# Performance work log

Measured on AMD Instinct MI355X. Metric: run time of the kernel, lower is better.

Reference implementation:

```python
import jax, jax.numpy as jnp
import numpy as np

RESOLUTION = 128


def _bin_mask():
    # [4, 2] bool: corner i, dim d -> True if corner uses floor coord in dim d
    neigs = jnp.arange(4, dtype=jnp.int32)[:, None]
    dims = jnp.arange(2, dtype=jnp.int32)[None, :]
    return (neigs & (1 << dims)) == 0


def setup_inputs() -> dict:
    key = jax.random.key(0)
    k1, k2 = jax.random.split(key)
    batch = 65536
    res, map_num, feat_dim = RESOLUTION, 128, 8
    inputs = jax.random.uniform(k1, (batch, 2), dtype=jnp.float32)
    # xavier_uniform over [res^2, map_num*feat_dim]
    fan_in, fan_out = res * res, map_num * feat_dim
    bound = float(np.sqrt(6.0 / (fan_in + fan_out)))
    embeddings = jax.random.uniform(k2, (res * res, map_num * feat_dim),
                                    dtype=jnp.float32, minval=-bound, maxval=bound)
    return {"inputs": inputs, "embeddings": embeddings}


def reference(inputs, embeddings):
    res = RESOLUTION
    bin_mask = _bin_mask()                      # [4, 2]
    x = inputs * (res - 1)                      # [B, 2]
    xi = jnp.floor(x).astype(jnp.int32)         # [B, 2]
    xf = x - jax.lax.stop_gradient(jnp.floor(x))  # fractional part, grads flow via x
    xi = xi[:, None, :]                         # [B, 1, 2]
    xf = xf[:, None, :]                         # [B, 1, 2]
    neigs = jnp.where(bin_mask, xi, xi + 1)     # [B, 4, 2]
    ids = neigs[..., 0] * res + neigs[..., 1]   # [B, 4]
    neigs_features = embeddings[ids]            # [B, 4, D] irregular gather
    weights = jnp.where(bin_mask, 1.0 - xf, xf) # [B, 4, 2]
    w = jnp.prod(weights, axis=-1, keepdims=True)  # [B, 4, 1]
    return jnp.sum(neigs_features * w, axis=-2)    # [B, D]
```

## Files before the change

kernel.cpp:

```cpp
#include <hip/hip_runtime.h>

#define RES   128
#define FEAT  1024
#define NBINS (RES * RES)

__global__ __launch_bounds__(256)
void hist_kernel(const float* __restrict__ inputs, unsigned* __restrict__ hist, int N)
{
    int p = blockIdx.x * 256 + threadIdx.x;
    if (p >= N) return;
    int i0 = (int)floorf(inputs[2 * p + 0] * (float)(RES - 1));
    int i1 = (int)floorf(inputs[2 * p + 1] * (float)(RES - 1));
    atomicAdd(&hist[i0 * RES + i1], 1u);
}

__global__ __launch_bounds__(256)
void scan_kernel(unsigned* __restrict__ hist)
{
    __shared__ unsigned part[256];
    int t = threadIdx.x;
    int base = t * 64;
    unsigned s = 0;
    for (int k = 0; k < 64; ++k) s += hist[base + k];
    part[t] = s;
    __syncthreads();
    if (t == 0) {
        unsigned run = 0;
        for (int i = 0; i < 256; ++i) { unsigned v = part[i]; part[i] = run; run += v; }
    }
    __syncthreads();
    unsigned run = part[t];
    for (int k = 0; k < 64; ++k) { unsigned v = hist[base + k]; hist[base + k] = run; run += v; }
}

__global__ __launch_bounds__(256)
void scatter_kernel(const float* __restrict__ inputs, unsigned* __restrict__ hist,
                    unsigned* __restrict__ order, int N)
{
    int p = blockIdx.x * 256 + threadIdx.x;
    if (p >= N) return;
    int i0 = (int)floorf(inputs[2 * p + 0] * (float)(RES - 1));
    int i1 = (int)floorf(inputs[2 * p + 1] * (float)(RES - 1));
    unsigned pos = atomicAdd(&hist[i0 * RES + i1], 1u);
    order[pos] = (unsigned)p;
}

__global__ __launch_bounds__(256)
void DenseMap_sorted_kernel(const float* __restrict__ inputs,
                            const float* __restrict__ emb,
                            const unsigned* __restrict__ order,
                            float* __restrict__ out,
                            int N, int chunk)
{
    const int b = blockIdx.x;
    const int c = threadIdx.x;
    const int g = (chunk > 0) ? ((b & 7) * chunk + (b >> 3)) : b;

#pragma unroll
    for (int j = 0; j < 4; ++j) {
        const int s = g * 4 + j;
        if (s >= N) break;
        const int p = (int)order[s];

        const float x0 = inputs[2 * p + 0] * (float)(RES - 1);
        const float x1 = inputs[2 * p + 1] * (float)(RES - 1);
        const float f0 = floorf(x0);
        const float f1 = floorf(x1);
        const int   i0 = (int)f0;
        const int   i1 = (int)f1;
        const float xf0 = x0 - f0;
        const float xf1 = x1 - f1;

        const float w00 = (1.0f - xf0) * (1.0f - xf1);
        const float w01 = (1.0f - xf0) * xf1;
        const float w10 = xf0 * (1.0f - xf1);
        const float w11 = xf0 * xf1;

        const long base = (long)(i0 * RES + i1) * FEAT;
        const float4 a = ((const float4*)(emb + base))[c];
        const float4 bb = ((const float4*)(emb + base + FEAT))[c];
        const float4 gg = ((const float4*)(emb + base + (long)RES * FEAT))[c];
        const float4 h = ((const float4*)(emb + base + (long)RES * FEAT + FEAT))[c];

        float4 r;
        r.x = a.x * w00 + bb.x * w01 + gg.x * w10 + h.x * w11;
        r.y = a.y * w00 + bb.y * w01 + gg.y * w10 + h.y * w11;
        r.z = a.z * w00 + bb.z * w01 + gg.z * w10 + h.z * w11;
        r.w = a.w * w00 + bb.w * w01 + gg.w * w10 + h.w * w11;

        ((float4*)(out + (long)p * FEAT))[c] = r;
    }
}

__global__ __launch_bounds__(256)
void DenseMap_fallback_kernel(const float* __restrict__ inputs,
                              const float* __restrict__ emb,
                              float* __restrict__ out)
{
    const int p = blockIdx.x;
    const int c = threadIdx.x;

    const float x0 = inputs[2 * p + 0] * (float)(RES - 1);
    const float x1 = inputs[2 * p + 1] * (float)(RES - 1);
    const float f0 = floorf(x0);
    const float f1 = floorf(x1);
    const int   i0 = (int)f0;
    const int   i1 = (int)f1;
    const float xf0 = x0 - f0;
    const float xf1 = x1 - f1;

    const float w00 = (1.0f - xf0) * (1.0f - xf1);
    const float w01 = (1.0f - xf0) * xf1;
    const float w10 = xf0 * (1.0f - xf1);
    const float w11 = xf0 * xf1;

    const long base = (long)(i0 * RES + i1) * FEAT;
    const float4 a = ((const float4*)(emb + base))[c];
    const float4 b = ((const float4*)(emb + base + FEAT))[c];
    const float4 g = ((const float4*)(emb + base + (long)RES * FEAT))[c];
    const float4 h = ((const float4*)(emb + base + (long)RES * FEAT + FEAT))[c];

    float4 r;
    r.x = a.x * w00 + b.x * w01 + g.x * w10 + h.x * w11;
    r.y = a.y * w00 + b.y * w01 + g.y * w10 + h.y * w11;
    r.z = a.z * w00 + b.z * w01 + g.z * w10 + h.z * w11;
    r.w = a.w * w00 + b.w * w01 + g.w * w10 + h.w * w11;

    ((float4*)(out + (long)p * FEAT))[c] = r;
}

extern "C" void kernel_launch(void* const* d_in, const int* in_sizes, int n_in,
                              void* d_out, int out_size, void* d_ws, size_t ws_size,
                              hipStream_t stream)
{
    const float* inputs = (const float*)d_in[0];
    const float* emb    = (const float*)d_in[1];
    float*       out    = (float*)d_out;

    const int N = in_sizes[0] / 2;
    const size_t need = (size_t)(NBINS + N) * sizeof(unsigned);

    if (ws_size >= need) {
        unsigned* hist  = (unsigned*)d_ws;
        unsigned* order = hist + NBINS;

        hipMemsetAsync(hist, 0, NBINS * sizeof(unsigned), stream);
        hist_kernel<<<(N + 255) / 256, 256, 0, stream>>>(inputs, hist, N);
        scan_kernel<<<1, 256, 0, stream>>>(hist);
        scatter_kernel<<<(N + 255) / 256, 256, 0, stream>>>(inputs, hist, order, N);

        const int G = (N + 3) / 4;
        const int chunk = (G % 8 == 0) ? (G / 8) : 0;
        DenseMap_sorted_kernel<<<G, 256, 0, stream>>>(inputs, emb, order, out, N, chunk);
    } else {
        DenseMap_fallback_kernel<<<N, 256, 0, stream>>>(inputs, emb, out);
    }
}
```

Baseline: 388.6 us.

## Sort points in Morton order, batch eight points per block, use nontemporal stores

Sort keys change from row-major cell index to a Z-order (Morton) code, so consecutive sorted points are spatially local in both dimensions and reuse more embedding rows in cache. Each block now processes eight points instead of four and computes all indices and weights up front, so several gathers can be in flight at once. Output is written with nontemporal stores so it does not evict embedding lines from cache. The cost is more registers per thread and fewer blocks.

```diff
diff --git a/kernel.cpp b/kernel.cpp
--- a/kernel.cpp
+++ b/kernel.cpp
@@ -3,15 +3,32 @@
 #define RES   128
 #define FEAT  1024
 #define NBINS (RES * RES)
+#define PPB   8
+
+typedef float float4n __attribute__((ext_vector_type(4)));
+
+__device__ __forceinline__ unsigned part1by1(unsigned x)
+{
+    x &= 0x7F;
+    x = (x | (x << 4)) & 0x0F0F;
+    x = (x | (x << 2)) & 0x3333;
+    x = (x | (x << 1)) & 0x5555;
+    return x;
+}
+
+__device__ __forceinline__ unsigned cell_code(const float* __restrict__ inputs, int p)
+{
+    int i0 = (int)floorf(inputs[2 * p + 0] * (float)(RES - 1));
+    int i1 = (int)floorf(inputs[2 * p + 1] * (float)(RES - 1));
+    return (part1by1((unsigned)i0) << 1) | part1by1((unsigned)i1);
+}
 
 __global__ __launch_bounds__(256)
 void hist_kernel(const float* __restrict__ inputs, unsigned* __restrict__ hist, int N)
 {
     int p = blockIdx.x * 256 + threadIdx.x;
     if (p >= N) return;
-    int i0 = (int)floorf(inputs[2 * p + 0] * (float)(RES - 1));
-    int i1 = (int)floorf(inputs[2 * p + 1] * (float)(RES - 1));
-    atomicAdd(&hist[i0 * RES + i1], 1u);
+    atomicAdd(&hist[cell_code(inputs, p)], 1u);
 }
 
 __global__ __launch_bounds__(256)
@@ -39,9 +56,7 @@
 {
     int p = blockIdx.x * 256 + threadIdx.x;
     if (p >= N) return;
-    int i0 = (int)floorf(inputs[2 * p + 0] * (float)(RES - 1));
-    int i1 = (int)floorf(inputs[2 * p + 1] * (float)(RES - 1));
-    unsigned pos = atomicAdd(&hist[i0 * RES + i1], 1u);
+    unsigned pos = atomicAdd(&hist[cell_code(inputs, p)], 1u);
     order[pos] = (unsigned)p;
 }
 
@@ -55,40 +70,45 @@
     const int b = blockIdx.x;
     const int c = threadIdx.x;
     const int g = (chunk > 0) ? ((b & 7) * chunk + (b >> 3)) : b;
+    const int s0 = g * PPB;
+
+    long  base[PPB];
+    float W00[PPB], W01[PPB], W10[PPB], W11[PPB];
+    int   pp[PPB];
 
 #pragma unroll
-    for (int j = 0; j < 4; ++j) {
-        const int s = g * 4 + j;
-        if (s >= N) break;
-        const int p = (int)order[s];
+    for (int j = 0; j < PPB; ++j) {
+        const int s = s0 + j;
+        const int p = (s < N) ? (int)order[s] : -1;
+        pp[j] = p;
+        if (p >= 0) {
+            const float x0 = inputs[2 * p + 0] * (float)(RES - 1);
+            const float x1 = inputs[2 * p + 1] * (float)(RES - 1);
+            const float f0 = floorf(x0);
+            const float f1 = floorf(x1);
+            const float xf0 = x0 - f0;
+            const float xf1 = x1 - f1;
+            base[j] = (long)((int)f0 * RES + (int)f1) * FEAT;
+            W00[j] = (1.0f - xf0) * (1.0f - xf1);
+            W01[j] = (1.0f - xf0) * xf1;
+            W10[j] = xf0 * (1.0f - xf1);
+            W11[j] = xf0 * xf1;
+        }
+    }
 
-        const float x0 = inputs[2 * p + 0] * (float)(RES - 1);
-        const float x1 = inputs[2 * p + 1] * (float)(RES - 1);
-        const float f0 = floorf(x0);
-        const float f1 = floorf(x1);
-        const int   i0 = (int)f0;
-        const int   i1 = (int)f1;
-        const float xf0 = x0 - f0;
-        const float xf1 = x1 - f1;
+#pragma unroll
+    for (int j = 0; j < PPB; ++j) {
+        const int p = pp[j];
+        if (p < 0) continue;
+        const long bs = base[j];
+        const float4n a  = ((const float4n*)(emb + bs))[c];
+        const float4n bb = ((const float4n*)(emb + bs + FEAT))[c];
+        const float4n gg = ((const float4n*)(emb + bs + (long)RES * FEAT))[c];
+        const float4n hh = ((const float4n*)(emb + bs + (long)RES * FEAT + FEAT))[c];
 
-        const float w00 = (1.0f - xf0) * (1.0f - xf1);
-        const float w01 = (1.0f - xf0) * xf1;
-        const float w10 = xf0 * (1.0f - xf1);
-        const float w11 = xf0 * xf1;
+        float4n r = a * W00[j] + bb * W01[j] + gg * W10[j] + hh * W11[j];
 
-        const long base = (long)(i0 * RES + i1) * FEAT;
-        const float4 a = ((const float4*)(emb + base))[c];
-        const float4 bb = ((const float4*)(emb + base + FEAT))[c];
-        const float4 gg = ((const float4*)(emb + base + (long)RES * FEAT))[c];
-        const float4 h = ((const float4*)(emb + base + (long)RES * FEAT + FEAT))[c];
-
-        float4 r;
-        r.x = a.x * w00 + bb.x * w01 + gg.x * w10 + h.x * w11;
-        r.y = a.y * w00 + bb.y * w01 + gg.y * w10 + h.y * w11;
-        r.z = a.z * w00 + bb.z * w01 + gg.z * w10 + h.z * w11;
-        r.w = a.w * w00 + bb.w * w01 + gg.w * w10 + h.w * w11;
-
-        ((float4*)(out + (long)p * FEAT))[c] = r;
+        __builtin_nontemporal_store(r, (float4n*)(out + (long)p * FEAT) + c);
     }
 }
 
@@ -115,18 +135,13 @@
     const float w11 = xf0 * xf1;
 
     const long base = (long)(i0 * RES + i1) * FEAT;
-    const float4 a = ((const float4*)(emb + base))[c];
-    const float4 b = ((const float4*)(emb + base + FEAT))[c];
-    const float4 g = ((const float4*)(emb + base + (long)RES * FEAT))[c];
-    const float4 h = ((const float4*)(emb + base + (long)RES * FEAT + FEAT))[c];
+    const float4n a = ((const float4n*)(emb + base))[c];
+    const float4n b = ((const float4n*)(emb + base + FEAT))[c];
+    const float4n g = ((const float4n*)(emb + base + (long)RES * FEAT))[c];
+    const float4n h = ((const float4n*)(emb + base + (long)RES * FEAT + FEAT))[c];
 
-    float4 r;
-    r.x = a.x * w00 + b.x * w01 + g.x * w10 + h.x * w11;
-    r.y = a.y * w00 + b.y * w01 + g.y * w10 + h.y * w11;
-    r.z = a.z * w00 + b.z * w01 + g.z * w10 + h.z * w11;
-    r.w = a.w * w00 + b.w * w01 + g.w * w10 + h.w * w11;
-
-    ((float4*)(out + (long)p * FEAT))[c] = r;
+    float4n r = a * w00 + b * w01 + g * w10 + h * w11;
+    ((float4n*)(out + (long)p * FEAT))[c] = r;
 }
 
 extern "C" void kernel_launch(void* const* d_in, const int* in_sizes, int n_in,
@@ -144,12 +159,12 @@
         unsigned* hist  = (unsigned*)d_ws;
         unsigned* order = hist + NBINS;
 
-        hipMemsetAsync(hist, 0, NBINS * sizeof(unsigned), stream);
+        (void)hipMemsetAsync(hist, 0, NBINS * sizeof(unsigned), stream);
         hist_kernel<<<(N + 255) / 256, 256, 0, stream>>>(inputs, hist, N);
         scan_kernel<<<1, 256, 0, stream>>>(hist);
         scatter_kernel<<<(N + 255) / 256, 256, 0, stream>>>(inputs, hist, order, N);
 
-        const int G = (N + 3) / 4;
+        const int G = (N + PPB - 1) / PPB;
         const int chunk = (G % 8 == 0) ? (G / 8) : 0;
         DenseMap_sorted_kernel<<<G, 256, 0, stream>>>(inputs, emb, order, out, N, chunk);
     } else {
```

New measurement: 399.6 us. 2.8% more time.
